# Kernel tuning notes

Measured on AMD Instinct MI355X. Metric: run time of the kernel, lower is better.

Reference implementation:

```python
import jax, jax.numpy as jnp
import numpy as np
import math

EPS = 1e-10
LAMBDA = 0.0001
LN_2PI = math.log(2 * math.pi)
OUTPUT_DIM = 32
NUM_ROUTING = 3


def setup_inputs() -> dict:
    key = jax.random.key(0)
    k1, k2, k3 = jax.random.split(key, 3)
    b, Bkk, Cww, hh = 8, 288, 1152, 17
    votes = jax.random.uniform(k1, (b, Bkk, Cww, hh), dtype=jnp.float32)
    beta_v = jax.random.normal(k2, (1, OUTPUT_DIM, 1, 1), dtype=jnp.float32)
    beta_a = jax.random.normal(k3, (1, OUTPUT_DIM, 1), dtype=jnp.float32)
    return {"votes": votes, "beta_v": beta_v, "beta_a": beta_a}


def reference(votes, beta_v, beta_a):
    b, Bkk, Cww, hh = votes.shape
    C = OUTPUT_DIM
    w = int(math.sqrt(Cww // C))  # spatial width/height (w_x == w_y)
    V = votes[..., : hh - 1]            # (b, Bkk, Cww, hh-1) pose votes
    a_ = votes[..., hh - 1]             # (b, Bkk, Cww) input activations

    R = jnp.ones((b, Bkk, Cww), dtype=votes.dtype) / C
    mu = None
    a = None
    for i in range(NUM_ROUTING):
        # ---- M-step: weighted Gaussian (mu, sigma^2) per output capsule ----
        R = (R * a_)[..., None]                                   # (b, Bkk, Cww, 1)
        sum_R = R.sum(axis=1) + 0.0001                            # (b, Cww, 1)
        mu = ((R * V).sum(axis=1) / sum_R)[:, None]               # (b, 1, Cww, hh-1)
        V_minus_mu_sqr = (V - mu) ** 2 + EPS                      # (b, Bkk, Cww, hh-1)
        sigma_square = ((R * V_minus_mu_sqr).sum(axis=1) / sum_R)[:, None] + EPS  # (b,1,Cww,hh-1)
        log_sigma = jnp.log(jnp.sqrt(sigma_square) + EPS)         # (b, 1, Cww, hh-1)
        cost = (beta_v + log_sigma.reshape(b, C, -1, hh - 1)) * sum_R.reshape(b, C, -1, 1)
        a = jax.nn.sigmoid(LAMBDA * (beta_a - cost.sum(-1)))      # (b, C, w*w)
        a = a.reshape(b, Cww)
        # ---- E-step: responsibilities from new Gaussian + activations ----
        if i != NUM_ROUTING - 1:
            ln_p_j_h = -V_minus_mu_sqr / (2 * sigma_square) - log_sigma - 0.5 * LN_2PI
            p_j_h = jnp.exp(ln_p_j_h)                             # (b, Bkk, Cww, hh-1)
            ap = a[:, None, :] * p_j_h.sum(-1)                    # (b, Bkk, Cww)
            R = jax.lax.stop_gradient(ap / (ap.sum(axis=2, keepdims=True) + EPS) + EPS)

    mu_a = jnp.concatenate(
        [mu.reshape(b, C, w, w, hh - 1), a.reshape(b, C, w, w, 1)], axis=-1
    )  # (b, C, w, w, hh)
    R_out = R.reshape(b, Bkk, C, w, w)
    return mu_a, R_out, votes
```

## Files before the change

### kernel.cpp

```cpp
#include <hip/hip_runtime.h>

#define NB   8
#define BKK  288
#define CWW  1152
#define HH   17
#define EPSF 1e-10f
#define ICH  16
#define ISZ  18
#define JT   18
#define ECH  8
#define NECH 36

struct __attribute__((aligned(4))) f4u { float x, y, z, w; };


__global__ __launch_bounds__(256) void mpart_kernel(
    const float* __restrict__ votes,
    const float* __restrict__ rt_in,
    float* __restrict__ a_dense,
    float* __restrict__ p12,
    float* __restrict__ p0)
{
    const int x  = blockIdx.x;
    const int jt = x % JT;
    const int c  = (x / JT) % ICH;
    const int b  = x / (JT * ICH);
    const int t  = threadIdx.x;
    const int jl = t >> 2;
    const int h4 = t & 3;
    const int i0 = c * ISZ;

    const size_t rowe = (size_t)CWW * HH;
    const float* base = votes + ((size_t)b * BKK + i0) * rowe + jt * (64 * HH);
    const int voff = jl * HH + h4 * 4;
    const int aoff = jl * HH + 16;

    float s0 = 0.f;
    float s1x=0.f,s1y=0.f,s1z=0.f,s1w=0.f;
    float s2x=0.f,s2y=0.f,s2z=0.f,s2w=0.f;

    if (rt_in == nullptr) {
        #pragma unroll 6
        for (int i = 0; i < ISZ; i++) {
            const float* rec = base + (size_t)i * rowe;
            f4u v = *(const f4u*)(rec + voff);
            float a16 = rec[aoff];
            float rt = a16 * (1.f / 32.f);
            s0 += rt;
            s1x += rt*v.x; s2x += rt*v.x*v.x;
            s1y += rt*v.y; s2y += rt*v.y*v.y;
            s1z += rt*v.z; s2z += rt*v.z*v.z;
            s1w += rt*v.w; s2w += rt*v.w*v.w;
            if (h4 == 0)
                a_dense[((size_t)b*BKK + i0 + i)*CWW + jt*64 + jl] = a16;
        }
    } else {
        const float* rb = rt_in + ((size_t)b*BKK + i0)*CWW + jt*64 + jl;
        #pragma unroll 6
        for (int i = 0; i < ISZ; i++) {
            const float* rec = base + (size_t)i * rowe;
            f4u v = *(const f4u*)(rec + voff);
            float rt = rb[(size_t)i * CWW];
            s0 += rt;
            s1x += rt*v.x; s2x += rt*v.x*v.x;
            s1y += rt*v.y; s2y += rt*v.y*v.y;
            s1z += rt*v.z; s2z += rt*v.z*v.z;
            s1w += rt*v.w; s2w += rt*v.w*v.w;
        }
    }

    const int j = jt * 64 + jl;
    float* o = p12 + (((size_t)(b * CWW + j)) * ICH + c) * 32 + h4 * 4;
    *(float4*)o        = make_float4(s1x, s1y, s1z, s1w);
    *(float4*)(o + 16) = make_float4(s2x, s2y, s2z, s2w);
    if (h4 == 0) p0[((size_t)(b * CWW + j)) * ICH + c] = s0;
}

__global__ __launch_bounds__(256) void mfin_kernel(
    const float* __restrict__ p12,
    const float* __restrict__ p0,
    const float* __restrict__ beta_v,
    const float* __restrict__ beta_a,
    float* __restrict__ params,
    float* __restrict__ out_mua)
{
    const int wid  = (blockIdx.x * 256 + threadIdx.x) >> 6;
    const int lane = threadIdx.x & 63;
    const int h    = lane & 15;
    const int q    = lane >> 4;
    const int b    = wid / CWW;
    const int j    = wid - b * CWW;

    float s0 = 0.f, s1 = 0.f, s2 = 0.f;
    #pragma unroll
    for (int cc = 0; cc < 4; cc++) {
        int c = q * 4 + cc;
        const float* pp = p12 + ((size_t)wid * ICH + c) * 32;
        s1 += pp[h];
        s2 += pp[16 + h];
        s0 += p0[(size_t)wid * ICH + c];
    }
    s0 += __shfl_xor(s0, 16); s1 += __shfl_xor(s1, 16); s2 += __shfl_xor(s2, 16);
    s0 += __shfl_xor(s0, 32); s1 += __shfl_xor(s1, 32); s2 += __shfl_xor(s2, 32);

    float sumR  = s0 + 1e-4f;
    float mu    = s1 / sumR;
    float var   = s2 - 2.f * mu * s1 + mu * mu * s0 + EPSF * s0;
    var = fmaxf(var, 0.f);
    float sigsq = var / sumR + EPSF;
    float sig   = sqrtf(sigsq);
    float ls    = logf(sig + EPSF);
    float lssum = ls;
    lssum += __shfl_xor(lssum, 1);
    lssum += __shfl_xor(lssum, 2);
    lssum += __shfl_xor(lssum, 4);
    lssum += __shfl_xor(lssum, 8);
    const int c = j / 36;
    float cost = (16.f * beta_v[c] + lssum) * sumR;
    float aa   = 1.f / (1.f + expf(-1e-4f * (beta_a[c] - cost)));

    if (params) {
        if (q == 0) {
            float* p = params + (size_t)wid * 48;
            p[h]      = mu;
            p[16 + h] = 0.5f / sigsq;
            p[32 + h] = aa * 0.3989422804014327f / (sig + EPSF);
        }
    } else {
        float* o = out_mua + (size_t)wid * HH;
        if (q == 0) o[h] = mu;
        if (lane == 16) o[16] = aa;
    }
}

__global__ __launch_bounds__(256) void estepA_kernel(
    const float* __restrict__ votes,
    const float* __restrict__ params,
    float* __restrict__ p_arr,
    float* __restrict__ psum,
    float* __restrict__ copy_dst)
{
    __shared__ float wsum[4][ECH];
    const int x  = blockIdx.x;
    const int jt = x % JT;
    const int ic = (x / JT) % NECH;
    const int b  = x / (JT * NECH);
    const int t  = threadIdx.x;
    const int jl = t >> 2;
    const int h4 = t & 3;
    const int j  = jt * 64 + jl;
    const int i0 = ic * ECH;
    const int lane = t & 63, w = t >> 6;

    const float* pj4 = params + ((size_t)b * CWW + j) * 48 + h4 * 4;
    float4 pm = *(const float4*)(pj4);
    float4 pi = *(const float4*)(pj4 + 16);
    float4 pw = *(const float4*)(pj4 + 32);

    const size_t rowe = (size_t)CWW * HH;
    const float* base = votes + ((size_t)b * BKK + i0) * rowe + jt * (64 * HH);
    float* cbase = copy_dst ? copy_dst + ((size_t)b * BKK + i0) * rowe + jt * (64 * HH)
                            : nullptr;
    const int voff = jl * HH + h4 * 4;
    const int aoff = jl * HH + 16;

    #pragma unroll 4
    for (int i = 0; i < ECH; i++) {
        const float* rec = base + (size_t)i * rowe;
        f4u v = *(const f4u*)(rec + voff);
        float d, pj = 0.f;
        d = v.x - pm.x; pj += pw.x * __expf(-(d * d + EPSF) * pi.x);
        d = v.y - pm.y; pj += pw.y * __expf(-(d * d + EPSF) * pi.y);
        d = v.z - pm.z; pj += pw.z * __expf(-(d * d + EPSF) * pi.z);
        d = v.w - pm.w; pj += pw.w * __expf(-(d * d + EPSF) * pi.w);
        pj += __shfl_xor(pj, 1);
        pj += __shfl_xor(pj, 2);
        if (h4 == 0)
            p_arr[((size_t)b * BKK + i0 + i) * CWW + j] = pj;
        if (cbase) {
            float* crec = cbase + (size_t)i * rowe;
            *(f4u*)(crec + voff) = v;
            if (h4 == 0) crec[aoff] = rec[aoff];
        }
        float rs = pj;
        rs += __shfl_xor(rs, 4);
        rs += __shfl_xor(rs, 8);
        rs += __shfl_xor(rs, 16);
        rs += __shfl_xor(rs, 32);
        if (lane == 0) wsum[w][i] = rs;
    }
    __syncthreads();
    if (t < ECH) {
        float s = wsum[0][t] + wsum[1][t] + wsum[2][t] + wsum[3][t];
        psum[((size_t)b * BKK + i0 + t) * JT + jt] = s;
    }
}

__global__ __launch_bounds__(256) void estepB_kernel(
    const float* __restrict__ p_arr,
    const float* __restrict__ psum,
    const float* __restrict__ a_dense,
    float* __restrict__ rt_ws,
    float* __restrict__ r_out)
{
    const int bi = blockIdx.x;
    const int t  = threadIdx.x;
    const float* ps = psum + (size_t)bi * JT;
    float s = 0.f;
    #pragma unroll
    for (int k = 0; k < JT; k++) s += ps[k];
    float inv = 1.f / (s + EPSF);
    const size_t base = (size_t)bi * CWW;
    for (int j = t; j < CWW; j += 256) {
        float r = p_arr[base + j] * inv + EPSF;
        rt_ws[base + j] = r * a_dense[base + j];
        if (r_out) r_out[base + j] = r;
    }
}

__global__ __launch_bounds__(256) void copy4_kernel(
    const float4* __restrict__ src, float4* __restrict__ dst, int n)
{
    int idx = blockIdx.x * 256 + threadIdx.x;
    if (idx < n) dst[idx] = src[idx];
}

extern "C" void kernel_launch(void* const* d_in, const int* in_sizes, int n_in,
                              void* d_out, int out_size, void* d_ws, size_t ws_size,
                              hipStream_t stream)
{
    const float* votes  = (const float*)d_in[0];
    const float* beta_v = (const float*)d_in[1];
    const float* beta_a = (const float*)d_in[2];
    float* out       = (float*)d_out;
    float* out_mua   = out;
    float* out_R     = out + (size_t)NB * CWW * HH;
    float* out_votes = out_R + (size_t)NB * BKK * CWW;

    const size_t n_adense = (size_t)NB * BKK * CWW;
    const size_t n_rt     = n_adense;
    const size_t n_p      = n_adense;
    const size_t n_psum   = (size_t)NB * BKK * JT;
    const size_t n_p12    = (size_t)NB * CWW * ICH * 32;
    const size_t n_p0     = (size_t)NB * CWW * ICH;
    const size_t n_params = (size_t)NB * CWW * 48;
    const size_t need = (n_adense + n_rt + n_p + n_psum + n_p12 + n_p0 + n_params)
                        * sizeof(float);

    float* scr;
    bool fused;
    if (ws_size >= need) { scr = (float*)d_ws; fused = true; }
    else                 { scr = out_votes;    fused = false; }
    float* a_dense = scr;
    float* rt_ws   = a_dense + n_adense;
    float* p_arr   = rt_ws + n_rt;
    float* psum    = p_arr + n_p;
    float* p12     = psum + n_psum;
    float* p0      = p12 + n_p12;
    float* params  = p0 + n_p0;

    dim3 blk(256);
    dim3 gmp(NB * ICH * JT);
    dim3 gmf(NB * CWW / 4);
    dim3 gea(NB * NECH * JT);
    dim3 geb(NB * BKK);

    mpart_kernel<<<gmp, blk, 0, stream>>>(votes, nullptr, a_dense, p12, p0);
    mfin_kernel<<<gmf, blk, 0, stream>>>(p12, p0, beta_v, beta_a, params, nullptr);
    estepA_kernel<<<gea, blk, 0, stream>>>(votes, params, p_arr, psum, nullptr);
    estepB_kernel<<<geb, blk, 0, stream>>>(p_arr, psum, a_dense, rt_ws, nullptr);
    mpart_kernel<<<gmp, blk, 0, stream>>>(votes, rt_ws, a_dense, p12, p0);
    mfin_kernel<<<gmf, blk, 0, stream>>>(p12, p0, beta_v, beta_a, params, nullptr);
    estepA_kernel<<<gea, blk, 0, stream>>>(votes, params, p_arr, psum,
                                           fused ? out_votes : nullptr);
    estepB_kernel<<<geb, blk, 0, stream>>>(p_arr, psum, a_dense, rt_ws, out_R);
    mpart_kernel<<<gmp, blk, 0, stream>>>(votes, rt_ws, a_dense, p12, p0);
    mfin_kernel<<<gmf, blk, 0, stream>>>(p12, p0, beta_v, beta_a, nullptr, out_mua);

    if (!fused) {
        int n4 = (int)((size_t)NB * BKK * CWW * HH / 4);
        copy4_kernel<<<dim3((n4 + 255) / 256), blk, 0, stream>>>(
            (const float4*)votes, (float4*)out_votes, n4);
    }
}
```

Before: 512.5 us.

## Fuse E-step normalization into M-step partial reduction and coalesce votes copy

Drops the separate estepB pass that wrote the rt_ws and R arrays. A tiny rowsum kernel now computes the inverse row sums, and the M-step partial kernel rebuilds R from p_arr, rsinv and a_dense on the fly, writing out_R with nontemporal stores. This removes a full read/write pass over several large intermediate arrays per routing iteration. It also halves the number of i-chunks (ICH from 16 to 8, 36 rows each) to shrink the partial-sum buffers, and rewrites the votes copy in estepA as contiguous vector nontemporal stores.

```diff
diff --git a/kernel.cpp b/kernel.cpp
--- a/kernel.cpp
+++ b/kernel.cpp
@@ -5,21 +5,25 @@
 #define CWW  1152
 #define HH   17
 #define EPSF 1e-10f
-#define ICH  16
-#define ISZ  18
+#define ICH  8
+#define ISZ  36
 #define JT   18
 #define ECH  8
 #define NECH 36
 
 struct __attribute__((aligned(4))) f4u { float x, y, z, w; };
+typedef float v4f __attribute__((ext_vector_type(4)));
 
 
 __global__ __launch_bounds__(256) void mpart_kernel(
     const float* __restrict__ votes,
-    const float* __restrict__ rt_in,
-    float* __restrict__ a_dense,
+    const float* __restrict__ p_arr,
+    const float* __restrict__ rsinv,
+    const float* __restrict__ a_dense,
+    float* __restrict__ a_out,
     float* __restrict__ p12,
-    float* __restrict__ p0)
+    float* __restrict__ p0,
+    float* __restrict__ r_out)
 {
     const int x  = blockIdx.x;
     const int jt = x % JT;
@@ -34,12 +38,14 @@
     const float* base = votes + ((size_t)b * BKK + i0) * rowe + jt * (64 * HH);
     const int voff = jl * HH + h4 * 4;
     const int aoff = jl * HH + 16;
+    const size_t dbase = ((size_t)b * BKK + i0) * CWW + jt * 64 + jl;
+    const int bi0 = b * BKK + i0;
 
     float s0 = 0.f;
     float s1x=0.f,s1y=0.f,s1z=0.f,s1w=0.f;
     float s2x=0.f,s2y=0.f,s2z=0.f,s2w=0.f;
 
-    if (rt_in == nullptr) {
+    if (p_arr == nullptr) {
         #pragma unroll 6
         for (int i = 0; i < ISZ; i++) {
             const float* rec = base + (size_t)i * rowe;
@@ -51,21 +57,25 @@
             s1y += rt*v.y; s2y += rt*v.y*v.y;
             s1z += rt*v.z; s2z += rt*v.z*v.z;
             s1w += rt*v.w; s2w += rt*v.w*v.w;
-            if (h4 == 0)
-                a_dense[((size_t)b*BKK + i0 + i)*CWW + jt*64 + jl] = a16;
+            if (h4 == 0) a_out[dbase + (size_t)i * CWW] = a16;
         }
     } else {
-        const float* rb = rt_in + ((size_t)b*BKK + i0)*CWW + jt*64 + jl;
         #pragma unroll 6
         for (int i = 0; i < ISZ; i++) {
             const float* rec = base + (size_t)i * rowe;
             f4u v = *(const f4u*)(rec + voff);
-            float rt = rb[(size_t)i * CWW];
+            float pv = p_arr[dbase + (size_t)i * CWW];
+            float av = a_dense[dbase + (size_t)i * CWW];
+            float ri = rsinv[bi0 + i];
+            float rr = fmaf(pv, ri, EPSF);
+            float rt = rr * av;
             s0 += rt;
             s1x += rt*v.x; s2x += rt*v.x*v.x;
             s1y += rt*v.y; s2y += rt*v.y*v.y;
             s1z += rt*v.z; s2z += rt*v.z*v.z;
             s1w += rt*v.w; s2w += rt*v.w*v.w;
+            if (r_out && h4 == 0)
+                __builtin_nontemporal_store(rr, r_out + dbase + (size_t)i * CWW);
         }
     }
 
@@ -93,8 +103,8 @@
 
     float s0 = 0.f, s1 = 0.f, s2 = 0.f;
     #pragma unroll
-    for (int cc = 0; cc < 4; cc++) {
-        int c = q * 4 + cc;
+    for (int cc = 0; cc < ICH / 4; cc++) {
+        int c = q + cc * 4;
         const float* pp = p12 + ((size_t)wid * ICH + c) * 32;
         s1 += pp[h];
         s2 += pp[16 + h];
@@ -159,10 +169,11 @@
 
     const size_t rowe = (size_t)CWW * HH;
     const float* base = votes + ((size_t)b * BKK + i0) * rowe + jt * (64 * HH);
-    float* cbase = copy_dst ? copy_dst + ((size_t)b * BKK + i0) * rowe + jt * (64 * HH)
-                            : nullptr;
     const int voff = jl * HH + h4 * 4;
-    const int aoff = jl * HH + 16;
+
+    const v4f* vt4 = (const v4f*)votes;
+    v4f* ot4 = (v4f*)copy_dst;
+    const size_t fb0 = (((size_t)b * BKK + i0) * rowe + jt * (64 * HH)) >> 2;
 
     #pragma unroll 4
     for (int i = 0; i < ECH; i++) {
@@ -177,11 +188,17 @@
         pj += __shfl_xor(pj, 2);
         if (h4 == 0)
             p_arr[((size_t)b * BKK + i0 + i) * CWW + j] = pj;
-        if (cbase) {
-            float* crec = cbase + (size_t)i * rowe;
-            *(f4u*)(crec + voff) = v;
-            if (h4 == 0) crec[aoff] = rec[aoff];
-        }
+
+        if (copy_dst) {
+            size_t fb = fb0 + (size_t)i * (rowe >> 2);
+            v4f c0 = vt4[fb + t];
+            __builtin_nontemporal_store(c0, ot4 + fb + t);
+            if (t < 16) {
+                v4f c1 = vt4[fb + 256 + t];
+                __builtin_nontemporal_store(c1, ot4 + fb + 256 + t);
+            }
+        }
+
         float rs = pj;
         rs += __shfl_xor(rs, 4);
         rs += __shfl_xor(rs, 8);
@@ -196,25 +213,16 @@
     }
 }
 
-__global__ __launch_bounds__(256) void estepB_kernel(
-    const float* __restrict__ p_arr,
-    const float* __restrict__ psum,
-    const float* __restrict__ a_dense,
-    float* __restrict__ rt_ws,
-    float* __restrict__ r_out)
-{
-    const int bi = blockIdx.x;
-    const int t  = threadIdx.x;
-    const float* ps = psum + (size_t)bi * JT;
-    float s = 0.f;
-    #pragma unroll
-    for (int k = 0; k < JT; k++) s += ps[k];
-    float inv = 1.f / (s + EPSF);
-    const size_t base = (size_t)bi * CWW;
-    for (int j = t; j < CWW; j += 256) {
-        float r = p_arr[base + j] * inv + EPSF;
-        rt_ws[base + j] = r * a_dense[base + j];
-        if (r_out) r_out[base + j] = r;
+__global__ __launch_bounds__(256) void rowsum_kernel(
+    const float* __restrict__ psum, float* __restrict__ rsinv)
+{
+    int bi = blockIdx.x * 256 + threadIdx.x;
+    if (bi < NB * BKK) {
+        const float* ps = psum + (size_t)bi * JT;
+        float s = 0.f;
+        #pragma unroll
+        for (int k = 0; k < JT; k++) s += ps[k];
+        rsinv[bi] = 1.f / (s + EPSF);
     }
 }
 
@@ -238,13 +246,13 @@
     float* out_votes = out_R + (size_t)NB * BKK * CWW;
 
     const size_t n_adense = (size_t)NB * BKK * CWW;
-    const size_t n_rt     = n_adense;
     const size_t n_p      = n_adense;
     const size_t n_psum   = (size_t)NB * BKK * JT;
+    const size_t n_rsinv  = (size_t)NB * BKK;
     const size_t n_p12    = (size_t)NB * CWW * ICH * 32;
     const size_t n_p0     = (size_t)NB * CWW * ICH;
     const size_t n_params = (size_t)NB * CWW * 48;
-    const size_t need = (n_adense + n_rt + n_p + n_psum + n_p12 + n_p0 + n_params)
+    const size_t need = (n_adense + n_p + n_psum + n_rsinv + n_p12 + n_p0 + n_params)
                         * sizeof(float);
 
     float* scr;
@@ -252,10 +260,10 @@
     if (ws_size >= need) { scr = (float*)d_ws; fused = true; }
     else                 { scr = out_votes;    fused = false; }
     float* a_dense = scr;
-    float* rt_ws   = a_dense + n_adense;
-    float* p_arr   = rt_ws + n_rt;
+    float* p_arr   = a_dense + n_adense;
     float* psum    = p_arr + n_p;
-    float* p12     = psum + n_psum;
+    float* rsinv   = psum + n_psum;
+    float* p12     = rsinv + n_rsinv;
     float* p0      = p12 + n_p12;
     float* params  = p0 + n_p0;
 
@@ -263,18 +271,21 @@
     dim3 gmp(NB * ICH * JT);
     dim3 gmf(NB * CWW / 4);
     dim3 gea(NB * NECH * JT);
-    dim3 geb(NB * BKK);
-
-    mpart_kernel<<<gmp, blk, 0, stream>>>(votes, nullptr, a_dense, p12, p0);
+    dim3 grs((NB * BKK + 255) / 256);
+
+    mpart_kernel<<<gmp, blk, 0, stream>>>(votes, nullptr, nullptr, nullptr,
+                                          a_dense, p12, p0, nullptr);
     mfin_kernel<<<gmf, blk, 0, stream>>>(p12, p0, beta_v, beta_a, params, nullptr);
     estepA_kernel<<<gea, blk, 0, stream>>>(votes, params, p_arr, psum, nullptr);
-    estepB_kernel<<<geb, blk, 0, stream>>>(p_arr, psum, a_dense, rt_ws, nullptr);
-    mpart_kernel<<<gmp, blk, 0, stream>>>(votes, rt_ws, a_dense, p12, p0);
+    rowsum_kernel<<<grs, blk, 0, stream>>>(psum, rsinv);
+    mpart_kernel<<<gmp, blk, 0, stream>>>(votes, p_arr, rsinv, a_dense,
+                                          nullptr, p12, p0, nullptr);
     mfin_kernel<<<gmf, blk, 0, stream>>>(p12, p0, beta_v, beta_a, params, nullptr);
     estepA_kernel<<<gea, blk, 0, stream>>>(votes, params, p_arr, psum,
                                            fused ? out_votes : nullptr);
-    estepB_kernel<<<geb, blk, 0, stream>>>(p_arr, psum, a_dense, rt_ws, out_R);
-    mpart_kernel<<<gmp, blk, 0, stream>>>(votes, rt_ws, a_dense, p12, p0);
+    rowsum_kernel<<<grs, blk, 0, stream>>>(psum, rsinv);
+    mpart_kernel<<<gmp, blk, 0, stream>>>(votes, p_arr, rsinv, a_dense,
+                                          nullptr, p12, p0, out_R);
     mfin_kernel<<<gmf, blk, 0, stream>>>(p12, p0, beta_v, beta_a, nullptr, out_mua);
 
     if (!fused) {
```

Result: faster. 455.1 us (-11.2%).
